# Optimization experiments

Measured on AMD Instinct MI355X. Metric: run time of the kernel, lower is better.

The kernel has to match this reference:

```python
import jax, jax.numpy as jnp
import numpy as np

N = 10000      # nodes
E = 160000     # edges (avg degree 16)
D = 128        # channels
H = 4          # heads
C = 128        # per-head dim (PyG: out_channels per head = channels)
HC = H * C
EPS_SOFTMAX = 1e-16
EPS_NORM = 1e-5


def setup_inputs() -> dict:
    key = jax.random.key(0)
    ks = jax.random.split(key, 12)
    s = 1.0 / np.sqrt(D)
    sb = 1.0 / np.sqrt(3 * D)
    return {
        "x": jax.random.normal(ks[0], (N, D), jnp.float32),
        "edge_index": jax.random.randint(ks[1], (2, E), 0, N, dtype=jnp.int64),
        "Wq": jax.random.normal(ks[2], (D, HC), jnp.float32) * s,
        "bq": jnp.zeros((HC,), jnp.float32),
        "Wk": jax.random.normal(ks[3], (D, HC), jnp.float32) * s,
        "bk": jnp.zeros((HC,), jnp.float32),
        "Wv": jax.random.normal(ks[4], (D, HC), jnp.float32) * s,
        "bv": jnp.zeros((HC,), jnp.float32),
        "Wskip": jax.random.normal(ks[5], (D, D), jnp.float32) * s,
        "bskip": jnp.zeros((D,), jnp.float32),
        "Wbeta": jax.random.normal(ks[6], (3 * D,), jnp.float32) * sb,  # lin_beta, bias=False
        "gn_weight": jnp.ones((D,), jnp.float32),
        "gn_bias": jnp.zeros((D,), jnp.float32),
        "gn_mean_scale": jnp.ones((D,), jnp.float32),
    }


def reference(x, edge_index, Wq, bq, Wk, bk, Wv, bv, Wskip, bskip, Wbeta,
              gn_weight, gn_bias, gn_mean_scale):
    n = x.shape[0]
    src, dst = edge_index[0], edge_index[1]  # messages flow src(j) -> dst(i)

    # Projections [N,H,C]
    q = (x @ Wq + bq).reshape(n, H, C)
    k = (x @ Wk + bk).reshape(n, H, C)
    v = (x @ Wv + bv).reshape(n, H, C)

    # Per-edge attention logits [E,H]
    alpha = jnp.einsum('ehc,ehc->eh', q[dst], k[src]) / jnp.sqrt(jnp.float32(C))

    # Segment softmax over incoming edges of each dst node
    amax = jax.ops.segment_max(alpha, dst, num_segments=n)       # [N,H]
    amax = jnp.where(jnp.isfinite(amax), amax, 0.0)
    ex = jnp.exp(alpha - amax[dst])                              # [E,H]
    denom = jax.ops.segment_sum(ex, dst, num_segments=n)         # [N,H]
    attn = ex / (denom[dst] + EPS_SOFTMAX)                       # [E,H]

    # Weighted scatter-aggregate, then mean over heads (concat=False)
    msgs = attn[:, :, None] * v[src]                             # [E,H,C]
    out = jax.ops.segment_sum(msgs, dst, num_segments=n)         # [N,H,C]
    out = out.mean(axis=1)                                       # [N,D]

    # Beta-gated skip (PyG: beta = sigmoid(lin_beta([out, x_r, out - x_r])))
    skip = x @ Wskip + bskip
    beta = jax.nn.sigmoid(jnp.concatenate([out, skip, out - skip], axis=-1) @ Wbeta)
    beta = beta[:, None]
    out = beta * skip + (1.0 - beta) * out

    # GraphNorm (single graph): (x - mean_scale*mean) / sqrt(var + eps) * w + b
    mean = out.mean(axis=0)
    centered = out - gn_mean_scale * mean
    var = (centered * centered).mean(axis=0)
    out = gn_weight * centered / jnp.sqrt(var + EPS_NORM) + gn_bias

    # GELU (exact) + residual (shapes match); dropout is identity in eval
    out = jax.nn.gelu(out, approximate=False)
    return out + x
```

## Files before the change

kernel.cpp:

```cpp
#include <hip/hip_runtime.h>
#include <hip/hip_bf16.h>
#include <math.h>

#define D_DIM 128
#define HC_DIM 512
#define CAP 128
#define REP 4

typedef __attribute__((ext_vector_type(8))) short bf16x8;
typedef __attribute__((ext_vector_type(4))) float f32x4;
typedef __attribute__((ext_vector_type(2))) float f32x2;
typedef __attribute__((ext_vector_type(2))) _Float16 h16x2;

static __device__ __forceinline__ unsigned short f2bf(float f) {
  unsigned u = __float_as_uint(f);
  unsigned r = (u + 0x7fffu + ((u >> 16) & 1u)) >> 16;
  return (unsigned short)r;
}
static __device__ __forceinline__ float bflo(unsigned u) {
  return __uint_as_float(u << 16);
}
static __device__ __forceinline__ float bfhi(unsigned u) {
  return __uint_as_float(u & 0xffff0000u);
}

__global__ void prep_kernel(const float* __restrict__ x,
                            const float* __restrict__ Wq, const float* __restrict__ Wk,
                            const float* __restrict__ Wv, const float* __restrict__ Wskip,
                            const float* __restrict__ bq, const float* __restrict__ bk,
                            const float* __restrict__ bv, const float* __restrict__ bskip,
                            unsigned short* __restrict__ xb,
                            unsigned short* __restrict__ wcat,
                            float* __restrict__ bcat,
                            int* __restrict__ zbase, int zwords, int N) {
  int t = blockIdx.x * 256 + threadIdx.x;
  int X4 = N * 32;
  if (t < X4) {
    float4 f = *(const float4*)&x[t * 4];
    ushort4 o;
    o.x = f2bf(f.x); o.y = f2bf(f.y); o.z = f2bf(f.z); o.w = f2bf(f.w);
    *(ushort4*)&xb[t * 4] = o;
  } else if (t < X4 + 1664 * 128) {
    int widx = t - X4;
    if (widx < 3 * 65536) {
      int segi = widx >> 16;
      int r = widx & 65535;
      int kk = r >> 9;
      int m = r & 511;
      const float* W = (segi == 0) ? Wq : (segi == 1) ? Wk : Wv;
      wcat[(size_t)(segi * 512 + m) * 128 + kk] = f2bf(W[kk * 512 + m]);
    } else {
      int r = widx - 3 * 65536;
      int kk = r >> 7;
      int m = r & 127;
      wcat[(size_t)(1536 + m) * 128 + kk] = f2bf(Wskip[kk * 128 + m]);
    }
  } else if (t < X4 + 1664 * 128 + 1664) {
    int b = t - X4 - 1664 * 128;
    bcat[b] = (b < 512) ? bq[b] : (b < 1024) ? bk[b - 512]
            : (b < 1536) ? bv[b - 1024] : bskip[b - 1536];
  } else if (t < X4 + 1664 * 128 + 1664 + zwords) {
    zbase[t - X4 - 1664 * 128 - 1664] = 0;
  }
}

__global__ __launch_bounds__(256) void gemm_mfma_kernel(
    const unsigned short* __restrict__ Xb, const unsigned short* __restrict__ Wt,
    const float* __restrict__ bcat, unsigned short* __restrict__ qb,
    unsigned short* __restrict__ kf, unsigned char* __restrict__ v8,
    float* __restrict__ skip,
    const int* __restrict__ src, const int* __restrict__ dst,
    int* __restrict__ cnt, int* __restrict__ bsrc, int N, int E) {
  const int tid = threadIdx.x;
  {
    int nblk = gridDim.x * gridDim.y;
    int lb = blockIdx.y * gridDim.x + blockIdx.x;
    int per = (E + nblk - 1) / nblk;
    int e0 = lb * per;
    int e1 = min(e0 + per, E);
    for (int e = e0 + tid; e < e1; e += 256) {
      int d = dst[e];
      int p = atomicAdd(&cnt[d], 1);
      if (p < CAP) bsrc[d * CAP + p] = src[e];
    }
  }
  const int wave = tid >> 6, lane = tid & 63;
  const int l16 = lane & 15, quad = lane >> 4;
  const int row0 = (blockIdx.x * 4 + wave) * 64;
  const int col0 = blockIdx.y * 64;

  const unsigned short* xrow[4];
#pragma unroll
  for (int i = 0; i < 4; ++i) {
    int r = row0 + i * 16 + l16;
    if (r >= N) r = N - 1;
    xrow[i] = Xb + (size_t)r * 128;
  }
  const unsigned short* wrow[4];
  float bias[4];
#pragma unroll
  for (int j = 0; j < 4; ++j) {
    int c = col0 + j * 16 + l16;
    wrow[j] = Wt + (size_t)c * 128;
    bias[j] = bcat[c];
  }

  f32x4 acc[4][4] = {};
#pragma unroll
  for (int kk = 0; kk < 4; ++kk) {
    int k0 = kk * 32 + quad * 8;
    bf16x8 a[4], b[4];
#pragma unroll
    for (int i = 0; i < 4; ++i) a[i] = *(const bf16x8*)(xrow[i] + k0);
#pragma unroll
    for (int j = 0; j < 4; ++j) b[j] = *(const bf16x8*)(wrow[j] + k0);
#pragma unroll
    for (int i = 0; i < 4; ++i)
#pragma unroll
      for (int j = 0; j < 4; ++j)
        acc[i][j] = __builtin_amdgcn_mfma_f32_16x16x32_bf16(a[i], b[j], acc[i][j], 0, 0, 0);
  }

  const int kind = (col0 < 512) ? 0 : (col0 < 1024) ? 1 : (col0 < 1536) ? 2 : 3;
#pragma unroll
  for (int i = 0; i < 4; ++i) {
#pragma unroll
    for (int reg = 0; reg < 4; ++reg) {
      int r = row0 + i * 16 + quad * 4 + reg;
      if (r < N) {
#pragma unroll
        for (int j = 0; j < 4; ++j) {
          int cidx = col0 + j * 16 + l16;
          float val = acc[i][j][reg] + bias[j];
          if (kind == 0) {
            qb[(size_t)r * 512 + cidx] = f2bf(val);
          } else if (kind == 1) {
            _Float16 hv = (_Float16)val;
            kf[(size_t)r * 512 + cidx - 512] = *(unsigned short*)&hv;
          } else if (kind == 2) {
            int pk = __builtin_amdgcn_cvt_pk_fp8_f32(val, val, 0, false);
            v8[(size_t)r * 512 + cidx - 1024] = (unsigned char)pk;
          } else {
            skip[(size_t)r * 128 + cidx - 1536] = val;
          }
        }
      }
    }
  }
}

__global__ __launch_bounds__(256) void attn_combine_kernel(
    const unsigned short* __restrict__ qb, const unsigned short* __restrict__ kf,
    const unsigned char* __restrict__ v8, const int* __restrict__ cnt,
    const int* __restrict__ bsrc, const float* __restrict__ skip,
    const float* __restrict__ Wbeta, float* __restrict__ out2,
    float* __restrict__ colsum, float* __restrict__ colsq, int N) {
  __shared__ int eL[4][CAP];
  __shared__ float redS[4][128];
  __shared__ float redQ[4][128];
  int tid = threadIdx.x;
  int w = tid >> 6, lane = tid & 63;
  int node = blockIdx.x * 4 + w;
  bool nv = node < N;
  int nc = nv ? node : (N - 1);
  int g = lane >> 4, j = lane & 15;

  int count = nv ? min(cnt[nc], CAP) : 0;
  const int* bp = bsrc + (size_t)nc * CAP;
  for (int i = lane; i < count; i += 64) eL[w][i] = bp[i];

  const float qscale = 0.08838834764831845f * 1.4426950408889634f;
  h16x2 qh[4][4];
#pragma unroll
  for (int h = 0; h < 4; ++h) {
    int4 qi = *(const int4*)(qb + (size_t)nc * 512 + h * 128 + j * 8);
    qh[h][0][0] = (_Float16)(bflo(qi.x) * qscale); qh[h][0][1] = (_Float16)(bfhi(qi.x) * qscale);
    qh[h][1][0] = (_Float16)(bflo(qi.y) * qscale); qh[h][1][1] = (_Float16)(bfhi(qi.y) * qscale);
    qh[h][2][0] = (_Float16)(bflo(qi.z) * qscale); qh[h][2][1] = (_Float16)(bfhi(qi.z) * qscale);
    qh[h][3][0] = (_Float16)(bflo(qi.w) * qscale); qh[h][3][1] = (_Float16)(bfhi(qi.w) * qscale);
  }

  float o[4][8];
  float lsum[4];
#pragma unroll
  for (int h = 0; h < 4; ++h) {
    lsum[h] = 0.f;
#pragma unroll
    for (int r = 0; r < 8; ++r) o[h][r] = 0.f;
  }

  if (count > 0) {
    int e = eL[w][(g < count) ? g : 0];
    uint4 kw[4]; uint2 vw[4];
    {
      const unsigned short* kbe = kf + (size_t)e * 512 + j * 8;
      const unsigned char* vbe = v8 + (size_t)e * 512 + j * 8;
#pragma unroll
      for (int h = 0; h < 4; ++h) {
        kw[h] = *(const uint4*)(kbe + h * 128);
        vw[h] = *(const uint2*)(vbe + h * 128);
      }
    }
    for (int idx = 0; idx < count; idx += 4) {
      int rem = count - idx;
      int nrem = rem - 4;
      int en = (nrem > 0) ? eL[w][idx + 4 + ((g < nrem) ? g : 0)] : e;
      uint4 kwn[4]; uint2 vwn[4];
      {
        const unsigned short* kbe = kf + (size_t)en * 512 + j * 8;
        const unsigned char* vbe = v8 + (size_t)en * 512 + j * 8;
#pragma unroll
        for (int h = 0; h < 4; ++h) {
          kwn[h] = *(const uint4*)(kbe + h * 128);
          vwn[h] = *(const uint2*)(vbe + h * 128);
        }
      }
      bool act = (g < rem);
#pragma unroll
      for (int h = 0; h < 4; ++h) {
        float p = __builtin_amdgcn_fdot2(qh[h][0], *(h16x2*)&kw[h].x, 0.f, false);
        p = __builtin_amdgcn_fdot2(qh[h][1], *(h16x2*)&kw[h].y, p, false);
        p = __builtin_amdgcn_fdot2(qh[h][2], *(h16x2*)&kw[h].z, p, false);
        p = __builtin_amdgcn_fdot2(qh[h][3], *(h16x2*)&kw[h].w, p, false);
        p += __shfl_xor(p, 1);
        p += __shfl_xor(p, 2);
        p += __shfl_xor(p, 4);
        p += __shfl_xor(p, 8);
        float a = act ? p : -1e30f;
        float wgt = exp2f(a);
        f32x2 v01 = __builtin_amdgcn_cvt_pk_f32_fp8(vw[h].x, false);
        f32x2 v23 = __builtin_amdgcn_cvt_pk_f32_fp8(vw[h].x, true);
        f32x2 v45 = __builtin_amdgcn_cvt_pk_f32_fp8(vw[h].y, false);
        f32x2 v67 = __builtin_amdgcn_cvt_pk_f32_fp8(vw[h].y, true);
        lsum[h] += wgt;
        o[h][0] += wgt * v01.x; o[h][1] += wgt * v01.y;
        o[h][2] += wgt * v23.x; o[h][3] += wgt * v23.y;
        o[h][4] += wgt * v45.x; o[h][5] += wgt * v45.y;
        o[h][6] += wgt * v67.x; o[h][7] += wgt * v67.y;
        kw[h] = kwn[h]; vw[h] = vwn[h];
      }
      e = en;
    }
  }
  float am[8];
#pragma unroll
  for (int r = 0; r < 8; ++r) am[r] = 0.f;
#pragma unroll
  for (int h = 0; h < 4; ++h) {
#pragma unroll
    for (int r = 0; r < 8; ++r) {
      o[h][r] += __shfl_xor(o[h][r], 16);
      o[h][r] += __shfl_xor(o[h][r], 32);
    }
    lsum[h] += __shfl_xor(lsum[h], 16);
    lsum[h] += __shfl_xor(lsum[h], 32);
    float inv = 0.25f / (lsum[h] + 1e-16f);
#pragma unroll
    for (int r = 0; r < 8; ++r) am[r] += o[h][r] * inv;
  }

  float4 sl = *(const float4*)&skip[(size_t)nc * 128 + j * 8];
  float4 sh = *(const float4*)&skip[(size_t)nc * 128 + j * 8 + 4];
  float4 wal = *(const float4*)&Wbeta[j * 8];
  float4 wah = *(const float4*)&Wbeta[j * 8 + 4];
  float4 wbl = *(const float4*)&Wbeta[128 + j * 8];
  float4 wbh = *(const float4*)&Wbeta[128 + j * 8 + 4];
  float4 wcl = *(const float4*)&Wbeta[256 + j * 8];
  float4 wch = *(const float4*)&Wbeta[256 + j * 8 + 4];
  float p = am[0] * wal.x + sl.x * wbl.x + (am[0] - sl.x) * wcl.x
          + am[1] * wal.y + sl.y * wbl.y + (am[1] - sl.y) * wcl.y
          + am[2] * wal.z + sl.z * wbl.z + (am[2] - sl.z) * wcl.z
          + am[3] * wal.w + sl.w * wbl.w + (am[3] - sl.w) * wcl.w
          + am[4] * wah.x + sh.x * wbh.x + (am[4] - sh.x) * wch.x
          + am[5] * wah.y + sh.y * wbh.y + (am[5] - sh.y) * wch.y
          + am[6] * wah.z + sh.z * wbh.z + (am[6] - sh.z) * wch.z
          + am[7] * wah.w + sh.w * wbh.w + (am[7] - sh.w) * wch.w;
  p += __shfl_xor(p, 1); p += __shfl_xor(p, 2);
  p += __shfl_xor(p, 4); p += __shfl_xor(p, 8);
  float beta = 1.f / (1.f + __expf(-p));
  float ob = 1.f - beta;
  float vm = nv ? 1.f : 0.f;
  float oc0 = (beta * sl.x + ob * am[0]) * vm;
  float oc1 = (beta * sl.y + ob * am[1]) * vm;
  float oc2 = (beta * sl.z + ob * am[2]) * vm;
  float oc3 = (beta * sl.w + ob * am[3]) * vm;
  float oc4 = (beta * sh.x + ob * am[4]) * vm;
  float oc5 = (beta * sh.y + ob * am[5]) * vm;
  float oc6 = (beta * sh.z + ob * am[6]) * vm;
  float oc7 = (beta * sh.w + ob * am[7]) * vm;

  if (g == 0) {
    float4 lo; lo.x = oc0; lo.y = oc1; lo.z = oc2; lo.w = oc3;
    float4 hi; hi.x = oc4; hi.y = oc5; hi.z = oc6; hi.w = oc7;
    if (nv) {
      *(float4*)&out2[(size_t)node * 128 + j * 8] = lo;
      *(float4*)&out2[(size_t)node * 128 + j * 8 + 4] = hi;
    }
    *(float4*)&redS[w][j * 8] = lo;
    *(float4*)&redS[w][j * 8 + 4] = hi;
    float4 ql; ql.x = oc0 * oc0; ql.y = oc1 * oc1; ql.z = oc2 * oc2; ql.w = oc3 * oc3;
    float4 qh2; qh2.x = oc4 * oc4; qh2.y = oc5 * oc5; qh2.z = oc6 * oc6; qh2.w = oc7 * oc7;
    *(float4*)&redQ[w][j * 8] = ql;
    *(float4*)&redQ[w][j * 8 + 4] = qh2;
  }
  __syncthreads();
  if (w == 0) {
    int c = lane * 2;
    float s0 = redS[0][c] + redS[1][c] + redS[2][c] + redS[3][c];
    float s1 = redS[0][c + 1] + redS[1][c + 1] + redS[2][c + 1] + redS[3][c + 1];
    float q0 = redQ[0][c] + redQ[1][c] + redQ[2][c] + redQ[3][c];
    float q1 = redQ[0][c + 1] + redQ[1][c + 1] + redQ[2][c + 1] + redQ[3][c + 1];
    int slot = (blockIdx.x & (REP - 1)) * 128;
    atomicAdd(&colsum[slot + c], s0);
    atomicAdd(&colsum[slot + c + 1], s1);
    atomicAdd(&colsq[slot + c], q0);
    atomicAdd(&colsq[slot + c + 1], q1);
  }
}

__global__ void final_kernel(const float* __restrict__ out2,
                             const float* __restrict__ colsum,
                             const float* __restrict__ colsq,
                             const float* __restrict__ gnw,
                             const float* __restrict__ gnb,
                             const float* __restrict__ gnms,
                             const float* __restrict__ x,
                             float* __restrict__ y, int total2, float invN) {
  int i = blockIdx.x * 256 + threadIdx.x;
  if (i < total2) {
    int c = (i & 63) * 2;
    float2 cs; cs.x = 0.f; cs.y = 0.f;
    float2 cq; cq.x = 0.f; cq.y = 0.f;
#pragma unroll
    for (int s = 0; s < REP; ++s) {
      float2 t = *(const float2*)&colsum[s * 128 + c];
      float2 u = *(const float2*)&colsq[s * 128 + c];
      cs.x += t.x; cs.y += t.y;
      cq.x += u.x; cq.y += u.y;
    }
    float2 gw = *(const float2*)&gnw[c];
    float2 gb = *(const float2*)&gnb[c];
    float2 gs = *(const float2*)&gnms[c];
    float mean0 = cs.x * invN, mean1 = cs.y * invN;
    float var0 = cq.x * invN - mean0 * mean0 * gs.x * (2.f - gs.x);
    float var1 = cq.y * invN - mean1 * mean1 * gs.y * (2.f - gs.y);
    float mul0 = gw.x / sqrtf(var0 + 1e-5f);
    float mul1 = gw.y / sqrtf(var1 + 1e-5f);
    float2 o = *(const float2*)&out2[i * 2];
    float2 xx = *(const float2*)&x[i * 2];
    float t0 = (o.x - gs.x * mean0) * mul0 + gb.x;
    float t1 = (o.y - gs.y * mean1) * mul1 + gb.y;
    float g0 = 0.5f * t0 * (1.f + erff(t0 * 0.70710678118654752f));
    float g1 = 0.5f * t1 * (1.f + erff(t1 * 0.70710678118654752f));
    float2 r; r.x = g0 + xx.x; r.y = g1 + xx.y;
    *(float2*)&y[i * 2] = r;
  }
}

extern "C" void kernel_launch(void* const* d_in, const int* in_sizes, int n_in,
                              void* d_out, int out_size, void* d_ws, size_t ws_size,
                              hipStream_t stream) {
  const float* x     = (const float*)d_in[0];
  const int*   ei    = (const int*)d_in[1];
  const float* Wq    = (const float*)d_in[2];
  const float* bq    = (const float*)d_in[3];
  const float* Wk    = (const float*)d_in[4];
  const float* bk    = (const float*)d_in[5];
  const float* Wv    = (const float*)d_in[6];
  const float* bv    = (const float*)d_in[7];
  const float* Wskip = (const float*)d_in[8];
  const float* bskip = (const float*)d_in[9];
  const float* Wbeta = (const float*)d_in[10];
  const float* gnw   = (const float*)d_in[11];
  const float* gnb   = (const float*)d_in[12];
  const float* gnms  = (const float*)d_in[13];

  const int N = in_sizes[0] / D_DIM;
  const int E = in_sizes[1] / 2;
  const int* src = ei;
  const int* dst = ei + E;

  char* p = (char*)d_ws;
  unsigned short* qb = (unsigned short*)p; p += (size_t)N * 512 * 2;
  unsigned short* kf = (unsigned short*)p; p += (size_t)N * 512 * 2;
  unsigned char*  v8 = (unsigned char*)p;  p += (size_t)N * 512;
  float*          skip = (float*)p;        p += (size_t)N * 128 * 4;
  float*          out2 = (float*)p;        p += (size_t)N * 128 * 4;
  int*   cnt    = (int*)p;   p += (size_t)N * 4;
  float* colsum = (float*)p; p += REP * 128 * 4;
  float* colsq  = (float*)p; p += REP * 128 * 4;
  int zwords = N + 2 * REP * 128;
  int* bsrc   = (int*)p;   p += (size_t)N * CAP * 4;
  unsigned short* wcat = (unsigned short*)p; p += (size_t)1664 * 128 * 2;
  float* bcat = (float*)p; p += 1664 * 4;
  unsigned short* xb = (unsigned short*)out2;

  int prepTotal = N * 32 + 1664 * 128 + 1664 + zwords;
  prep_kernel<<<(prepTotal + 255) / 256, 256, 0, stream>>>(
      x, Wq, Wk, Wv, Wskip, bq, bk, bv, bskip, xb, wcat, bcat, cnt, zwords, N);

  gemm_mfma_kernel<<<dim3(40, 26), 256, 0, stream>>>(
      xb, wcat, bcat, qb, kf, v8, skip, src, dst, cnt, bsrc, N, E);

  attn_combine_kernel<<<(N + 3) / 4, 256, 0, stream>>>(
      qb, kf, v8, cnt, bsrc, skip, Wbeta, out2, colsum, colsq, N);

  int total2 = N * D_DIM / 2;
  final_kernel<<<(total2 + 255) / 256, 256, 0, stream>>>(
      out2, colsum, colsq, gnw, gnb, gnms, x, (float*)d_out, total2, 1.f / (float)N);
}
```

Baseline: 179.1 us.

## Process one node per block, spreading edges across all four waves

```diff
diff --git a/kernel.cpp b/kernel.cpp
--- a/kernel.cpp
+++ b/kernel.cpp
@@ -5,7 +5,7 @@
 #define D_DIM 128
 #define HC_DIM 512
 #define CAP 128
-#define REP 4
+#define REP 16
 
 typedef __attribute__((ext_vector_type(8))) short bf16x8;
 typedef __attribute__((ext_vector_type(4))) float f32x4;
@@ -155,25 +155,24 @@
     const int* __restrict__ bsrc, const float* __restrict__ skip,
     const float* __restrict__ Wbeta, float* __restrict__ out2,
     float* __restrict__ colsum, float* __restrict__ colsq, int N) {
-  __shared__ int eL[4][CAP];
-  __shared__ float redS[4][128];
-  __shared__ float redQ[4][128];
+  __shared__ float oL[4][4][128];
+  __shared__ float lsumL[4][4];
   int tid = threadIdx.x;
   int w = tid >> 6, lane = tid & 63;
-  int node = blockIdx.x * 4 + w;
-  bool nv = node < N;
-  int nc = nv ? node : (N - 1);
+  int node = blockIdx.x;
   int g = lane >> 4, j = lane & 15;
-
-  int count = nv ? min(cnt[nc], CAP) : 0;
-  const int* bp = bsrc + (size_t)nc * CAP;
-  for (int i = lane; i < count; i += 64) eL[w][i] = bp[i];
+  int s = w * 4 + g;
+
+  int e0raw = bsrc[(size_t)node * CAP + s];
+  int count = min(cnt[node], CAP);
+  unsigned e0 = (unsigned)e0raw;
+  if (e0 >= (unsigned)N) e0 = 0;
 
   const float qscale = 0.08838834764831845f * 1.4426950408889634f;
   h16x2 qh[4][4];
 #pragma unroll
   for (int h = 0; h < 4; ++h) {
-    int4 qi = *(const int4*)(qb + (size_t)nc * 512 + h * 128 + j * 8);
+    int4 qi = *(const int4*)(qb + (size_t)node * 512 + h * 128 + j * 8);
     qh[h][0][0] = (_Float16)(bflo(qi.x) * qscale); qh[h][0][1] = (_Float16)(bfhi(qi.x) * qscale);
     qh[h][1][0] = (_Float16)(bflo(qi.y) * qscale); qh[h][1][1] = (_Float16)(bfhi(qi.y) * qscale);
     qh[h][2][0] = (_Float16)(bflo(qi.z) * qscale); qh[h][2][1] = (_Float16)(bfhi(qi.z) * qscale);
@@ -189,62 +188,55 @@
     for (int r = 0; r < 8; ++r) o[h][r] = 0.f;
   }
 
-  if (count > 0) {
-    int e = eL[w][(g < count) ? g : 0];
+  auto compute = [&](const uint4* kw, const uint2* vw, bool act) {
+#pragma unroll
+    for (int h = 0; h < 4; ++h) {
+      float p = __builtin_amdgcn_fdot2(qh[h][0], *(h16x2*)&kw[h].x, 0.f, false);
+      p = __builtin_amdgcn_fdot2(qh[h][1], *(h16x2*)&kw[h].y, p, false);
+      p = __builtin_amdgcn_fdot2(qh[h][2], *(h16x2*)&kw[h].z, p, false);
+      p = __builtin_amdgcn_fdot2(qh[h][3], *(h16x2*)&kw[h].w, p, false);
+      p += __shfl_xor(p, 1);
+      p += __shfl_xor(p, 2);
+      p += __shfl_xor(p, 4);
+      p += __shfl_xor(p, 8);
+      float a = act ? p : -1e30f;
+      float wgt = exp2f(a);
+      f32x2 v01 = __builtin_amdgcn_cvt_pk_f32_fp8(vw[h].x, false);
+      f32x2 v23 = __builtin_amdgcn_cvt_pk_f32_fp8(vw[h].x, true);
+      f32x2 v45 = __builtin_amdgcn_cvt_pk_f32_fp8(vw[h].y, false);
+      f32x2 v67 = __builtin_amdgcn_cvt_pk_f32_fp8(vw[h].y, true);
+      lsum[h] += wgt;
+      o[h][0] += wgt * v01.x; o[h][1] += wgt * v01.y;
+      o[h][2] += wgt * v23.x; o[h][3] += wgt * v23.y;
+      o[h][4] += wgt * v45.x; o[h][5] += wgt * v45.y;
+      o[h][6] += wgt * v67.x; o[h][7] += wgt * v67.y;
+    }
+  };
+
+  {
     uint4 kw[4]; uint2 vw[4];
-    {
-      const unsigned short* kbe = kf + (size_t)e * 512 + j * 8;
-      const unsigned char* vbe = v8 + (size_t)e * 512 + j * 8;
-#pragma unroll
-      for (int h = 0; h < 4; ++h) {
-        kw[h] = *(const uint4*)(kbe + h * 128);
-        vw[h] = *(const uint2*)(vbe + h * 128);
-      }
-    }
-    for (int idx = 0; idx < count; idx += 4) {
-      int rem = count - idx;
-      int nrem = rem - 4;
-      int en = (nrem > 0) ? eL[w][idx + 4 + ((g < nrem) ? g : 0)] : e;
-      uint4 kwn[4]; uint2 vwn[4];
-      {
-        const unsigned short* kbe = kf + (size_t)en * 512 + j * 8;
-        const unsigned char* vbe = v8 + (size_t)en * 512 + j * 8;
-#pragma unroll
-        for (int h = 0; h < 4; ++h) {
-          kwn[h] = *(const uint4*)(kbe + h * 128);
-          vwn[h] = *(const uint2*)(vbe + h * 128);
-        }
-      }
-      bool act = (g < rem);
-#pragma unroll
-      for (int h = 0; h < 4; ++h) {
-        float p = __builtin_amdgcn_fdot2(qh[h][0], *(h16x2*)&kw[h].x, 0.f, false);
-        p = __builtin_amdgcn_fdot2(qh[h][1], *(h16x2*)&kw[h].y, p, false);
-        p = __builtin_amdgcn_fdot2(qh[h][2], *(h16x2*)&kw[h].z, p, false);
-        p = __builtin_amdgcn_fdot2(qh[h][3], *(h16x2*)&kw[h].w, p, false);
-        p += __shfl_xor(p, 1);
-        p += __shfl_xor(p, 2);
-        p += __shfl_xor(p, 4);
-        p += __shfl_xor(p, 8);
-        float a = act ? p : -1e30f;
-        float wgt = exp2f(a);
-        f32x2 v01 = __builtin_amdgcn_cvt_pk_f32_fp8(vw[h].x, false);
-        f32x2 v23 = __builtin_amdgcn_cvt_pk_f32_fp8(vw[h].x, true);
-        f32x2 v45 = __builtin_amdgcn_cvt_pk_f32_fp8(vw[h].y, false);
-        f32x2 v67 = __builtin_amdgcn_cvt_pk_f32_fp8(vw[h].y, true);
-        lsum[h] += wgt;
-        o[h][0] += wgt * v01.x; o[h][1] += wgt * v01.y;
-        o[h][2] += wgt * v23.x; o[h][3] += wgt * v23.y;
-        o[h][4] += wgt * v45.x; o[h][5] += wgt * v45.y;
-        o[h][6] += wgt * v67.x; o[h][7] += wgt * v67.y;
-        kw[h] = kwn[h]; vw[h] = vwn[h];
-      }
-      e = en;
-    }
-  }
-  float am[8];
-#pragma unroll
-  for (int r = 0; r < 8; ++r) am[r] = 0.f;
+    const unsigned short* kbe = kf + (size_t)e0 * 512 + j * 8;
+    const unsigned char* vbe = v8 + (size_t)e0 * 512 + j * 8;
+#pragma unroll
+    for (int h = 0; h < 4; ++h) {
+      kw[h] = *(const uint4*)(kbe + h * 128);
+      vw[h] = *(const uint2*)(vbe + h * 128);
+    }
+    compute(kw, vw, s < count);
+  }
+  for (int idx = s + 16; idx < count; idx += 16) {
+    int e = bsrc[(size_t)node * CAP + idx];
+    uint4 kw[4]; uint2 vw[4];
+    const unsigned short* kbe = kf + (size_t)e * 512 + j * 8;
+    const unsigned char* vbe = v8 + (size_t)e * 512 + j * 8;
+#pragma unroll
+    for (int h = 0; h < 4; ++h) {
+      kw[h] = *(const uint4*)(kbe + h * 128);
+      vw[h] = *(const uint2*)(vbe + h * 128);
+    }
+    compute(kw, vw, true);
+  }
+
 #pragma unroll
   for (int h = 0; h < 4; ++h) {
 #pragma unroll
@@ -254,67 +246,53 @@
     }
     lsum[h] += __shfl_xor(lsum[h], 16);
     lsum[h] += __shfl_xor(lsum[h], 32);
-    float inv = 0.25f / (lsum[h] + 1e-16f);
-#pragma unroll
-    for (int r = 0; r < 8; ++r) am[r] += o[h][r] * inv;
-  }
-
-  float4 sl = *(const float4*)&skip[(size_t)nc * 128 + j * 8];
-  float4 sh = *(const float4*)&skip[(size_t)nc * 128 + j * 8 + 4];
-  float4 wal = *(const float4*)&Wbeta[j * 8];
-  float4 wah = *(const float4*)&Wbeta[j * 8 + 4];
-  float4 wbl = *(const float4*)&Wbeta[128 + j * 8];
-  float4 wbh = *(const float4*)&Wbeta[128 + j * 8 + 4];
-  float4 wcl = *(const float4*)&Wbeta[256 + j * 8];
-  float4 wch = *(const float4*)&Wbeta[256 + j * 8 + 4];
-  float p = am[0] * wal.x + sl.x * wbl.x + (am[0] - sl.x) * wcl.x
-          + am[1] * wal.y + sl.y * wbl.y + (am[1] - sl.y) * wcl.y
-          + am[2] * wal.z + sl.z * wbl.z + (am[2] - sl.z) * wcl.z
-          + am[3] * wal.w + sl.w * wbl.w + (am[3] - sl.w) * wcl.w
-          + am[4] * wah.x + sh.x * wbh.x + (am[4] - sh.x) * wch.x
-          + am[5] * wah.y + sh.y * wbh.y + (am[5] - sh.y) * wch.y
-          + am[6] * wah.z + sh.z * wbh.z + (am[6] - sh.z) * wch.z
-          + am[7] * wah.w + sh.w * wbh.w + (am[7] - sh.w) * wch.w;
-  p += __shfl_xor(p, 1); p += __shfl_xor(p, 2);
-  p += __shfl_xor(p, 4); p += __shfl_xor(p, 8);
-  float beta = 1.f / (1.f + __expf(-p));
-  float ob = 1.f - beta;
-  float vm = nv ? 1.f : 0.f;
-  float oc0 = (beta * sl.x + ob * am[0]) * vm;
-  float oc1 = (beta * sl.y + ob * am[1]) * vm;
-  float oc2 = (beta * sl.z + ob * am[2]) * vm;
-  float oc3 = (beta * sl.w + ob * am[3]) * vm;
-  float oc4 = (beta * sh.x + ob * am[4]) * vm;
-  float oc5 = (beta * sh.y + ob * am[5]) * vm;
-  float oc6 = (beta * sh.z + ob * am[6]) * vm;
-  float oc7 = (beta * sh.w + ob * am[7]) * vm;
-
+  }
   if (g == 0) {
-    float4 lo; lo.x = oc0; lo.y = oc1; lo.z = oc2; lo.w = oc3;
-    float4 hi; hi.x = oc4; hi.y = oc5; hi.z = oc6; hi.w = oc7;
-    if (nv) {
-      *(float4*)&out2[(size_t)node * 128 + j * 8] = lo;
-      *(float4*)&out2[(size_t)node * 128 + j * 8 + 4] = hi;
-    }
-    *(float4*)&redS[w][j * 8] = lo;
-    *(float4*)&redS[w][j * 8 + 4] = hi;
-    float4 ql; ql.x = oc0 * oc0; ql.y = oc1 * oc1; ql.z = oc2 * oc2; ql.w = oc3 * oc3;
-    float4 qh2; qh2.x = oc4 * oc4; qh2.y = oc5 * oc5; qh2.z = oc6 * oc6; qh2.w = oc7 * oc7;
-    *(float4*)&redQ[w][j * 8] = ql;
-    *(float4*)&redQ[w][j * 8 + 4] = qh2;
+#pragma unroll
+    for (int h = 0; h < 4; ++h) {
+      float4 lo; lo.x = o[h][0]; lo.y = o[h][1]; lo.z = o[h][2]; lo.w = o[h][3];
+      float4 hi; hi.x = o[h][4]; hi.y = o[h][5]; hi.z = o[h][6]; hi.w = o[h][7];
+      *(float4*)&oL[w][h][j * 8] = lo;
+      *(float4*)&oL[w][h][j * 8 + 4] = hi;
+    }
+    if (j == 0) {
+#pragma unroll
+      for (int h = 0; h < 4; ++h) lsumL[w][h] = lsum[h];
+    }
   }
   __syncthreads();
+
   if (w == 0) {
     int c = lane * 2;
-    float s0 = redS[0][c] + redS[1][c] + redS[2][c] + redS[3][c];
-    float s1 = redS[0][c + 1] + redS[1][c + 1] + redS[2][c + 1] + redS[3][c + 1];
-    float q0 = redQ[0][c] + redQ[1][c] + redQ[2][c] + redQ[3][c];
-    float q1 = redQ[0][c + 1] + redQ[1][c + 1] + redQ[2][c + 1] + redQ[3][c + 1];
+    float am0 = 0.f, am1 = 0.f;
+#pragma unroll
+    for (int h = 0; h < 4; ++h) {
+      float ls = lsumL[0][h] + lsumL[1][h] + lsumL[2][h] + lsumL[3][h];
+      float inv = 0.25f / (ls + 1e-16f);
+      float s0 = oL[0][h][c] + oL[1][h][c] + oL[2][h][c] + oL[3][h][c];
+      float s1 = oL[0][h][c + 1] + oL[1][h][c + 1] + oL[2][h][c + 1] + oL[3][h][c + 1];
+      am0 += s0 * inv;
+      am1 += s1 * inv;
+    }
+    float2 sk = *(const float2*)&skip[(size_t)node * 128 + c];
+    float2 wa = *(const float2*)&Wbeta[c];
+    float2 wb = *(const float2*)&Wbeta[128 + c];
+    float2 wc = *(const float2*)&Wbeta[256 + c];
+    float p = am0 * wa.x + sk.x * wb.x + (am0 - sk.x) * wc.x
+            + am1 * wa.y + sk.y * wb.y + (am1 - sk.y) * wc.y;
+#pragma unroll
+    for (int dmask = 1; dmask < 64; dmask <<= 1) p += __shfl_xor(p, dmask);
+    float beta = 1.f / (1.f + __expf(-p));
+    float ob = 1.f - beta;
+    float oc0 = beta * sk.x + ob * am0;
+    float oc1 = beta * sk.y + ob * am1;
+    float2 ov; ov.x = oc0; ov.y = oc1;
+    *(float2*)&out2[(size_t)node * 128 + c] = ov;
     int slot = (blockIdx.x & (REP - 1)) * 128;
-    atomicAdd(&colsum[slot + c], s0);
-    atomicAdd(&colsum[slot + c + 1], s1);
-    atomicAdd(&colsq[slot + c], q0);
-    atomicAdd(&colsq[slot + c + 1], q1);
+    atomicAdd(&colsum[slot + c], oc0);
+    atomicAdd(&colsum[slot + c + 1], oc1);
+    atomicAdd(&colsq[slot + c], oc0 * oc0);
+    atomicAdd(&colsq[slot + c + 1], oc1 * oc1);
   }
 }
 
@@ -402,7 +380,7 @@
   gemm_mfma_kernel<<<dim3(40, 26), 256, 0, stream>>>(
       xb, wcat, bcat, qb, kf, v8, skip, src, dst, cnt, bsrc, N, E);
 
-  attn_combine_kernel<<<(N + 3) / 4, 256, 0, stream>>>(
+  attn_combine_kernel<<<N, 256, 0, stream>>>(
       qb, kf, v8, cnt, bsrc, skip, Wbeta, out2, colsum, colsq, N);
 
   int total2 = N * D_DIM / 2;
```

New measurement: 190.3 us. 1.06x slower.
